# Performance work log

Measured on AMD Instinct MI355X. Metric: run time of the kernel, lower is better.

Reference implementation:

```python
import jax, jax.numpy as jnp
import numpy as np

BS, NQ, NTGT, NCLS, D = 16, 1024, 96, 4, 6
COST_CLASS, COST_BBOX = 1.0, 1.0
INF = jnp.float32(1e9)


def hungarian(cost):
    """Min-cost linear assignment (Jonker-Volgenant / e-maxx Hungarian).

    cost: (n, m) with n <= m. Returns (n,) int32: matched column for each row.
    Matches scipy.optimize.linear_sum_assignment's optimal assignment.
    """
    n, m = cost.shape
    # 1-indexed padded cost; row 0 / col 0 are virtual.
    a = jnp.zeros((n + 1, m + 1), jnp.float32).at[1:, 1:].set(cost.astype(jnp.float32))

    def assign_row(i, uvp):
        u, v, p = uvp  # p[j] = row matched to col j (0 = free)
        p = p.at[0].set(i)

        def dij_cond(c):
            _u, _v, _minv, _used, _way, j0 = c
            return p[j0] != 0

        def dij_body(c):
            u, v, minv, used, way, j0 = c
            used = used.at[j0].set(True)
            i0 = p[j0]
            cur = a[i0] - u[i0] - v                      # reduced costs, (m+1,)
            better = (cur < minv) & jnp.logical_not(used)
            minv = jnp.where(better, cur, minv)
            way = jnp.where(better, j0, way)
            masked = jnp.where(used, INF, minv)
            j1 = jnp.argmin(masked).astype(jnp.int32)
            delta = masked[j1]
            du = jnp.where(used, delta, jnp.float32(0))
            u = u.at[p].add(du)                          # u[p[j]] += delta for used j
            v = v - du
            minv = jnp.where(used, minv, minv - delta)
            return (u, v, minv, used, way, j1)

        minv0 = jnp.full(m + 1, INF, jnp.float32)
        used0 = jnp.zeros(m + 1, bool)
        way0 = jnp.zeros(m + 1, jnp.int32)
        u, v, _minv, _used, way, j0 = jax.lax.while_loop(
            dij_cond, dij_body, (u, v, minv0, used0, way0, jnp.int32(0)))

        def aug_cond(c):
            j0, _p = c
            return j0 != 0

        def aug_body(c):
            j0, p = c
            j1 = way[j0]
            p = p.at[j0].set(p[j1])
            return (j1, p)

        _, p = jax.lax.while_loop(aug_cond, aug_body, (j0, p))
        return (u, v, p)

    u0 = jnp.zeros(n + 1, jnp.float32)
    v0 = jnp.zeros(m + 1, jnp.float32)
    p0 = jnp.zeros(m + 1, jnp.int32)
    _, _, p = jax.lax.fori_loop(1, n + 1, assign_row, (u0, v0, p0))
    # invert: col4row[row] = col   (free cols / virtual col collapse into index 0)
    col4row = jnp.zeros(n + 1, jnp.int32).at[p[1:]].set(jnp.arange(1, m + 1, dtype=jnp.int32))
    return col4row[1:] - 1


def setup_inputs() -> dict:
    key = jax.random.key(0)
    k1, k2, k3, k4 = jax.random.split(key, 4)
    pred_logits = jax.random.normal(k1, (BS, NQ, NCLS), jnp.float32)
    pred_boxes = jax.random.uniform(k2, (BS, NQ, D), jnp.float32)
    labels = jax.random.randint(k3, (BS, NTGT), 0, NCLS, dtype=jnp.int32)
    control_points = jax.random.uniform(k4, (BS, NTGT, D), jnp.float32)
    return {"pred_logits": pred_logits, "pred_boxes": pred_boxes,
            "labels": labels, "control_points": control_points}


def reference(pred_logits, pred_boxes, labels, control_points):
    bs, nq, _ = pred_logits.shape
    ntgt = labels.shape[1]
    # cost matrix build (the memory-bound part)
    out_prob = jax.nn.softmax(pred_logits.reshape(bs * nq, -1), axis=-1)
    out_bbox = pred_boxes.reshape(bs * nq, -1)
    tgt_ids = labels.reshape(-1)
    tgt_bbox = control_points.reshape(bs * ntgt, -1)
    cost_class = -out_prob[:, tgt_ids]                              # (bs*nq, bs*ntgt)
    cost_bbox = jnp.abs(out_bbox[:, None, :] - tgt_bbox[None, :, :]).sum(-1)  # L1 cdist
    C = (COST_BBOX * cost_bbox + COST_CLASS * cost_class).reshape(bs, nq, bs * ntgt)

    # per-batch diagonal block -> Hungarian (targets as rows since ntgt <= nq)
    def per_batch(Cb, b):
        block = jax.lax.dynamic_slice(Cb, (0, b * ntgt), (nq, ntgt))  # (nq, ntgt)
        return hungarian(block.T)                                      # (ntgt,) matched query per target

    matched_query = jax.vmap(per_batch)(C, jnp.arange(bs, dtype=jnp.int32))
    return C, matched_query
```

## Files before the change

kernel.cpp:

```cpp
#include <hip/hip_runtime.h>


#define BSZ   16
#define NQ    1024
#define NTGT  96
#define NCLS  4
#define DD    6
#define NCOLS (BSZ * NTGT)
#define NROWS (BSZ * NQ)
#define LHINF 1e9f
#define NHB   16
#define ROWS_PER_BLK 8

typedef float f32x4 __attribute__((ext_vector_type(4)));

__device__ __forceinline__ float wave_fmin63(float x) {
    const int INF_I = __float_as_int(LHINF);
    int m;
    m = __builtin_amdgcn_update_dpp(INF_I, __float_as_int(x), 0x111, 0xf, 0xf, false);
    x = fminf(x, __int_as_float(m));
    m = __builtin_amdgcn_update_dpp(INF_I, __float_as_int(x), 0x112, 0xf, 0xf, false);
    x = fminf(x, __int_as_float(m));
    m = __builtin_amdgcn_update_dpp(INF_I, __float_as_int(x), 0x114, 0xf, 0xf, false);
    x = fminf(x, __int_as_float(m));
    m = __builtin_amdgcn_update_dpp(INF_I, __float_as_int(x), 0x118, 0xf, 0xf, false);
    x = fminf(x, __int_as_float(m));
    m = __builtin_amdgcn_update_dpp(INF_I, __float_as_int(x), 0x142, 0xf, 0xf, false);
    x = fminf(x, __int_as_float(m));
    m = __builtin_amdgcn_update_dpp(INF_I, __float_as_int(x), 0x143, 0xf, 0xf, false);
    x = fminf(x, __int_as_float(m));
    return x;
}

__device__ __forceinline__ float cost_elem6(const float* bx, const float* tv, float psel) {
    float cd = fabsf(bx[0] - tv[0]);
    cd += fabsf(bx[1] - tv[1]);
    cd += fabsf(bx[2] - tv[2]);
    cd += fabsf(bx[3] - tv[3]);
    cd += fabsf(bx[4] - tv[4]);
    cd += fabsf(bx[5] - tv[5]);
    return cd - psel;
}

__device__ __forceinline__ float4 softmax4(float4 lg) {
    const float mx = fmaxf(fmaxf(lg.x, lg.y), fmaxf(lg.z, lg.w));
    const float e0 = expf(lg.x - mx), e1 = expf(lg.y - mx);
    const float e2 = expf(lg.z - mx), e3 = expf(lg.w - mx);
    const float s = (e0 + e1) + (e2 + e3);
    return make_float4(e0 / s, e1 / s, e2 / s, e3 / s);
}

__global__ __launch_bounds__(256) void twsarg_kernel(
    const float* __restrict__ logits, const float* __restrict__ boxes,
    const int* __restrict__ labels, const float* __restrict__ tgt,
    float* __restrict__ tws, float* __restrict__ rowminv, int* __restrict__ rowarg)
{
    const int t = blockIdx.x;
    const int b = blockIdx.y;
    const int tr = b * NTGT + t;
    float tv[DD];
#pragma unroll
    for (int d = 0; d < DD; ++d) tv[d] = tgt[(size_t)tr * DD + d];
    const int cls = labels[tr];

    const int q4 = threadIdx.x * 4;
    const int row0 = b * NQ + q4;
    const float4* bx4 = (const float4*)(boxes + (size_t)row0 * DD);
    float bv[24];
#pragma unroll
    for (int c = 0; c < 6; ++c) {
        float4 f = bx4[c];
        bv[c * 4] = f.x; bv[c * 4 + 1] = f.y; bv[c * 4 + 2] = f.z; bv[c * 4 + 3] = f.w;
    }
    float o[4];
#pragma unroll
    for (int c = 0; c < 4; ++c) {
        const float4 p = softmax4(((const float4*)logits)[row0 + c]);
        const float ps = (cls == 0) ? p.x : (cls == 1) ? p.y : (cls == 2) ? p.z : p.w;
        o[c] = cost_elem6(bv + c * DD, tv, ps);
    }
    *((float4*)(tws + (size_t)tr * NQ + q4)) = make_float4(o[0], o[1], o[2], o[3]);

    float bvv = o[0]; int bj = q4;
    if (o[1] < bvv) { bvv = o[1]; bj = q4 + 1; }
    if (o[2] < bvv) { bvv = o[2]; bj = q4 + 2; }
    if (o[3] < bvv) { bvv = o[3]; bj = q4 + 3; }
#pragma unroll
    for (int off = 32; off > 0; off >>= 1) {
        const float ov = __shfl_down(bvv, off, 64);
        const int oj = __shfl_down(bj, off, 64);
        if (ov < bvv || (ov == bvv && oj < bj)) { bvv = ov; bj = oj; }
    }
    __shared__ float sv[4];
    __shared__ int sj[4];
    const int w = threadIdx.x >> 6;
    if ((threadIdx.x & 63) == 0) { sv[w] = bvv; sj[w] = bj; }
    __syncthreads();
    if (threadIdx.x == 0) {
        for (int i = 1; i < 4; ++i)
            if (sv[i] < bvv || (sv[i] == bvv && sj[i] < bj)) { bvv = sv[i]; bj = sj[i]; }
        rowminv[tr] = bvv; rowarg[tr] = bj;
    }
}

__global__ __launch_bounds__(384) void cost_kernel_fb(
    const float* __restrict__ logits, const float* __restrict__ boxes,
    const int* __restrict__ labels, const float* __restrict__ tgt,
    float* __restrict__ C)
{
    const int row = blockIdx.x;
    const int tid = threadIdx.x;
    const float4 pr = softmax4(*reinterpret_cast<const float4*>(logits + (size_t)row * NCLS));
    const float prr[4] = {pr.x, pr.y, pr.z, pr.w};
    float bx[DD];
#pragma unroll
    for (int d = 0; d < DD; ++d) bx[d] = boxes[(size_t)row * DD + d];
    const int colbase = tid * 4;
    const int4 lb = *reinterpret_cast<const int4*>(labels + colbase);
    const int cls[4] = {lb.x, lb.y, lb.z, lb.w};
    float tv[24];
    const float4* tg = reinterpret_cast<const float4*>(tgt + (size_t)colbase * DD);
#pragma unroll
    for (int d = 0; d < 6; ++d) {
        const float4 t4 = tg[d];
        tv[d * 4] = t4.x; tv[d * 4 + 1] = t4.y; tv[d * 4 + 2] = t4.z; tv[d * 4 + 3] = t4.w;
    }
    float o[4];
#pragma unroll
    for (int c = 0; c < 4; ++c) {
        const int cl = cls[c];
        const float ps = (cl == 0) ? prr[0] : (cl == 1) ? prr[1] : (cl == 2) ? prr[2] : prr[3];
        o[c] = cost_elem6(bx, tv + c * DD, ps);
    }
    *reinterpret_cast<float4*>(C + (size_t)row * NCOLS + colbase) =
        make_float4(o[0], o[1], o[2], o[3]);
}

__global__ __launch_bounds__(384) void fused_kernel(
    const float* __restrict__ tws, const float* __restrict__ logits,
    const float* __restrict__ boxes, const int* __restrict__ labels,
    const float* __restrict__ tgt,
    const float* __restrict__ rowminv, const int* __restrict__ rowarg,
    float* __restrict__ C, float* __restrict__ out_match, int warm)
{
    if (blockIdx.x >= NHB) {
        const int rb = (blockIdx.x - NHB) * ROWS_PER_BLK;
        const int tid = threadIdx.x;
        const int colbase = tid * 4;
        const int4 lb = ((const int4*)labels)[tid];
        const int cls[4] = {lb.x, lb.y, lb.z, lb.w};
        const float4* tg = (const float4*)(tgt + (size_t)colbase * DD);
        float tv[24];
#pragma unroll
        for (int c = 0; c < 6; ++c) {
            float4 f = tg[c];
            tv[c * 4] = f.x; tv[c * 4 + 1] = f.y; tv[c * 4 + 2] = f.z; tv[c * 4 + 3] = f.w;
        }
#pragma unroll
        for (int r = 0; r < ROWS_PER_BLK; ++r) {
            const int row = rb + r;
            const float4 pr = softmax4(((const float4*)logits)[row]);
            const float prr[4] = {pr.x, pr.y, pr.z, pr.w};
            const float* bp = boxes + (size_t)row * DD;
            float bx[DD];
#pragma unroll
            for (int d = 0; d < DD; ++d) bx[d] = bp[d];
            float o[4];
#pragma unroll
            for (int c = 0; c < 4; ++c) {
                const int cl = cls[c];
                const float ps = (cl == 0) ? prr[0] : (cl == 1) ? prr[1]
                               : (cl == 2) ? prr[2] : prr[3];
                o[c] = cost_elem6(bx, tv + c * DD, ps);
            }
            f32x4 ov;
            ov.x = o[0]; ov.y = o[1]; ov.z = o[2]; ov.w = o[3];
            __builtin_nontemporal_store(
                ov, (f32x4*)(C + (size_t)row * NCOLS + colbase));
        }
        return;
    }

    if (threadIdx.x >= 64) return;
    __builtin_amdgcn_s_setprio(2);
    const int b = blockIdx.x;
    const int lane = threadIdx.x;

    __shared__ float u_lds[NTGT + 1];
    __shared__ int   p_lds[NQ];
    __shared__ float dmark[NQ];
    __shared__ int   col_own[NQ];
    __shared__ int   ja_s[NTGT];
    __shared__ float um_s[NTGT];
    __shared__ int   pendf[NTGT];

    for (int t = lane; t < NQ; t += 64) { p_lds[t] = 0; col_own[t] = 0x7fffffff; }
    for (int t = lane; t < NTGT + 1; t += 64) u_lds[t] = 0.f;
    __builtin_amdgcn_wave_barrier();

    const int jbase = lane * 16;
    const float* Tb = tws + (size_t)b * NTGT * NQ;
    const float* Cstr = C + (size_t)b * NQ * NCOLS + b * NTGT;

    float v[16], Msel[16], msk[16];
    int way[16], p_reg[16];
#pragma unroll
    for (int k = 0; k < 16; ++k) v[k] = 0.f;

    if (warm) {
        for (int t = lane; t < NTGT; t += 64) {
            ja_s[t] = rowarg[b * NTGT + t];
            um_s[t] = rowminv[b * NTGT + t];
        }
        __builtin_amdgcn_wave_barrier();
        for (int t = lane; t < NTGT; t += 64)
            atomicMin(&col_own[ja_s[t]], t);
        __builtin_amdgcn_wave_barrier();
        for (int t = lane; t < NTGT; t += 64) {
            const int jt = ja_s[t];
            if (col_own[jt] == t) {
                p_lds[jt] = t + 1;
                u_lds[t + 1] = um_s[t];
                pendf[t] = 0;
            } else {
                pendf[t] = 1;
            }
        }
        __builtin_amdgcn_wave_barrier();
    } else {
        for (int t = lane; t < NTGT; t += 64) pendf[t] = 1;
        __builtin_amdgcn_wave_barrier();
    }

    for (int tt = 0; tt < NTGT; ++tt) {
        const int pending = __builtin_amdgcn_readfirstlane(pendf[tt]);
        if (!pending) continue;
        const int i = tt + 1;

        const int4* pl4 = (const int4*)(p_lds + jbase);
#pragma unroll
        for (int c = 0; c < 4; ++c) {
            int4 pp = pl4[c];
            p_reg[c * 4] = pp.x; p_reg[c * 4 + 1] = pp.y;
            p_reg[c * 4 + 2] = pp.z; p_reg[c * 4 + 3] = pp.w;
        }
#pragma unroll
        for (int k = 0; k < 16; ++k) { Msel[k] = LHINF; msk[k] = -LHINF; way[k] = 0; }
        unsigned used = 0u;
        int i0 = i; float Delta = 0.f; int j0cur = 0;
        bool domark = false; int markk = 0;
        float Dfinal = 0.f; int jfreem1 = 0;

        for (;;) {
            float av[16];
            if (warm) {
                const float4* rp = (const float4*)(Tb + (size_t)(i0 - 1) * NQ + jbase);
#pragma unroll
                for (int c = 0; c < 4; ++c) {
                    float4 f = rp[c];
                    av[c * 4] = f.x; av[c * 4 + 1] = f.y;
                    av[c * 4 + 2] = f.z; av[c * 4 + 3] = f.w;
                }
            } else {
                const float* cp = Cstr + (i0 - 1);
#pragma unroll
                for (int k = 0; k < 16; ++k) av[k] = cp[(size_t)(jbase + k) * NCOLS];
            }
            const float u_i0 = u_lds[i0];

#pragma unroll
            for (int k = 0; k < 16; ++k) {
                const bool mk = domark && (markk == k);
                Msel[k] = mk ? LHINF : Msel[k];
                msk[k]  = mk ? LHINF : msk[k];
            }
            used |= (domark ? (1u << markk) : 0u);

            const float c0 = Delta - u_i0;
            float lbv = LHINF; int lbk = 0; int lbp = 0;
#pragma unroll
            for (int k = 0; k < 16; ++k) {
                float cand = (av[k] - v[k]) + c0;
                cand = fmaxf(cand, msk[k]);
                const bool better = cand < Msel[k];
                way[k]  = better ? j0cur : way[k];
                Msel[k] = better ? cand : Msel[k];
                const bool b2 = Msel[k] < lbv;
                lbv = b2 ? Msel[k] : lbv;
                lbk = b2 ? k : lbk;
                lbp = b2 ? p_reg[k] : lbp;
            }
            const float red = wave_fmin63(lbv);
            const float gmin = __int_as_float(
                __builtin_amdgcn_readlane(__float_as_int(red), 63));
            const unsigned long long bal = __ballot(lbv == gmin);
            const int W = __builtin_amdgcn_readfirstlane((int)__builtin_ctzll(bal));
            const int lbjm1 = jbase + lbk;
            const int j1m1 = __builtin_amdgcn_readlane(lbjm1, W);
            const int i0n  = __builtin_amdgcn_readlane(lbp, W);
            const bool iswin = (lane == W);
            if (iswin) dmark[lbjm1] = lbv;
            domark = iswin; markk = lbk;
            if (i0n == 0) { Dfinal = gmin; jfreem1 = j1m1; break; }
            Delta = gmin; i0 = i0n; j0cur = j1m1 + 1;
        }

        __builtin_amdgcn_wave_barrier();
        float dmv[16];
        const float4* dm4 = (const float4*)(dmark + jbase);
#pragma unroll
        for (int c = 0; c < 4; ++c) {
            float4 f = dm4[c];
            dmv[c * 4] = f.x; dmv[c * 4 + 1] = f.y;
            dmv[c * 4 + 2] = f.z; dmv[c * 4 + 3] = f.w;
        }
#pragma unroll
        for (int k = 0; k < 16; ++k) {
            if ((used >> k) & 1u) {
                const float d = Dfinal - dmv[k];
                v[k] -= d;
                u_lds[p_reg[k]] += d;
            }
        }
        if (lane == 0) u_lds[i] += Dfinal;
        __builtin_amdgcn_wave_barrier();

        int j0m1 = jfreem1;
        for (;;) {
            const int kk = j0m1 & 15;
            const int owner = __builtin_amdgcn_readfirstlane(j0m1 >> 4);
            int s0 = (kk & 1) ? way[1]  : way[0];
            int s1 = (kk & 1) ? way[3]  : way[2];
            int s2 = (kk & 1) ? way[5]  : way[4];
            int s3 = (kk & 1) ? way[7]  : way[6];
            int s4 = (kk & 1) ? way[9]  : way[8];
            int s5 = (kk & 1) ? way[11] : way[10];
            int s6 = (kk & 1) ? way[13] : way[12];
            int s7 = (kk & 1) ? way[15] : way[14];
            int t0 = (kk & 2) ? s1 : s0;
            int t1 = (kk & 2) ? s3 : s2;
            int t2 = (kk & 2) ? s5 : s4;
            int t3 = (kk & 2) ? s7 : s6;
            int q0 = (kk & 4) ? t1 : t0;
            int q1 = (kk & 4) ? t3 : t2;
            int wsel = (kk & 8) ? q1 : q0;
            const int jn = __builtin_amdgcn_readlane(wsel, owner);
            const int pv = (jn == 0) ? i : p_lds[jn - 1];
            if (lane == 0) p_lds[j0m1] = pv;
            __builtin_amdgcn_wave_barrier();
            if (jn == 0) break;
            j0m1 = jn - 1;
        }
    }

    for (int t = lane; t < NQ; t += 64) {
        const int r = p_lds[t];
        if (r > 0) out_match[b * NTGT + r - 1] = (float)t;
    }
}

extern "C" void kernel_launch(void* const* d_in, const int* in_sizes, int n_in,
                              void* d_out, int out_size, void* d_ws, size_t ws_size,
                              hipStream_t stream) {
    const float* logits = (const float*)d_in[0];
    const float* boxes  = (const float*)d_in[1];
    const int*   labels = (const int*)d_in[2];
    const float* tgt    = (const float*)d_in[3];

    float* C = (float*)d_out;
    float* out_match = C + (size_t)NROWS * NCOLS;

    const size_t tws_e = (size_t)NCOLS * NQ;
    const size_t rmv_e = (size_t)NCOLS;
    const size_t need = (tws_e + rmv_e * 2) * sizeof(float);

    if (d_ws != nullptr && ws_size >= need) {
        float* tws     = (float*)d_ws;
        float* rowminv = tws + tws_e;
        int*   rowarg  = (int*)(rowminv + rmv_e);
        twsarg_kernel<<<dim3(NTGT, BSZ), 256, 0, stream>>>(
            logits, boxes, labels, tgt, tws, rowminv, rowarg);
        fused_kernel<<<NHB + NROWS / ROWS_PER_BLK, 384, 0, stream>>>(
            tws, logits, boxes, labels, tgt, rowminv, rowarg, C, out_match, 1);
    } else {
        cost_kernel_fb<<<NROWS, 384, 0, stream>>>(logits, boxes, labels, tgt, C);
        fused_kernel<<<NHB, 64, 0, stream>>>(
            nullptr, logits, boxes, labels, tgt, nullptr, nullptr, C, out_match, 0);
    }
}
```

Measured before the change: 167.7 us.

## Split fused cost-write/Hungarian kernel into separate sequential kernels

Breaks the fused kernel, which ran 16 Hungarian blocks alongside the C-writing blocks, into a standalone C-writing kernel followed by a separate Hungarian kernel launched with 64 threads per block. This removes the idle 320 threads and the priority hack in the Hungarian blocks, and lets the Hungarian waves run without competing for bandwidth or CUs with the C stores. In exchange it loses the overlap between the serial assignment work and the memory-bound C write, and adds a kernel launch.

```diff
diff --git a/kernel.cpp b/kernel.cpp
--- a/kernel.cpp
+++ b/kernel.cpp
@@ -9,7 +9,6 @@
 #define NCOLS (BSZ * NTGT)
 #define NROWS (BSZ * NQ)
 #define LHINF 1e9f
-#define NHB   16
 #define ROWS_PER_BLK 8
 
 typedef float f32x4 __attribute__((ext_vector_type(4)));
@@ -100,6 +99,47 @@
         for (int i = 1; i < 4; ++i)
             if (sv[i] < bvv || (sv[i] == bvv && sj[i] < bj)) { bvv = sv[i]; bj = sj[i]; }
         rowminv[tr] = bvv; rowarg[tr] = bj;
+    }
+}
+
+__global__ __launch_bounds__(384) void cwrite_kernel(
+    const float* __restrict__ logits, const float* __restrict__ boxes,
+    const int* __restrict__ labels, const float* __restrict__ tgt,
+    float* __restrict__ C)
+{
+    const int rb = blockIdx.x * ROWS_PER_BLK;
+    const int tid = threadIdx.x;
+    const int colbase = tid * 4;
+    const int4 lb = ((const int4*)labels)[tid];
+    const int cls[4] = {lb.x, lb.y, lb.z, lb.w};
+    const float4* tg = (const float4*)(tgt + (size_t)colbase * DD);
+    float tv[24];
+#pragma unroll
+    for (int c = 0; c < 6; ++c) {
+        float4 f = tg[c];
+        tv[c * 4] = f.x; tv[c * 4 + 1] = f.y; tv[c * 4 + 2] = f.z; tv[c * 4 + 3] = f.w;
+    }
+#pragma unroll
+    for (int r = 0; r < ROWS_PER_BLK; ++r) {
+        const int row = rb + r;
+        const float4 pr = softmax4(((const float4*)logits)[row]);
+        const float prr[4] = {pr.x, pr.y, pr.z, pr.w};
+        const float* bp = boxes + (size_t)row * DD;
+        float bx[DD];
+#pragma unroll
+        for (int d = 0; d < DD; ++d) bx[d] = bp[d];
+        float o[4];
+#pragma unroll
+        for (int c = 0; c < 4; ++c) {
+            const int cl = cls[c];
+            const float ps = (cl == 0) ? prr[0] : (cl == 1) ? prr[1]
+                           : (cl == 2) ? prr[2] : prr[3];
+            o[c] = cost_elem6(bx, tv + c * DD, ps);
+        }
+        f32x4 ov;
+        ov.x = o[0]; ov.y = o[1]; ov.z = o[2]; ov.w = o[3];
+        __builtin_nontemporal_store(
+            ov, (f32x4*)(C + (size_t)row * NCOLS + colbase));
     }
 }
 
@@ -136,53 +176,11 @@
         make_float4(o[0], o[1], o[2], o[3]);
 }
 
-__global__ __launch_bounds__(384) void fused_kernel(
-    const float* __restrict__ tws, const float* __restrict__ logits,
-    const float* __restrict__ boxes, const int* __restrict__ labels,
-    const float* __restrict__ tgt,
+__global__ __launch_bounds__(64) void hung_kernel(
+    const float* __restrict__ tws,
     const float* __restrict__ rowminv, const int* __restrict__ rowarg,
-    float* __restrict__ C, float* __restrict__ out_match, int warm)
+    const float* __restrict__ C, float* __restrict__ out_match, int warm)
 {
-    if (blockIdx.x >= NHB) {
-        const int rb = (blockIdx.x - NHB) * ROWS_PER_BLK;
-        const int tid = threadIdx.x;
-        const int colbase = tid * 4;
-        const int4 lb = ((const int4*)labels)[tid];
-        const int cls[4] = {lb.x, lb.y, lb.z, lb.w};
-        const float4* tg = (const float4*)(tgt + (size_t)colbase * DD);
-        float tv[24];
-#pragma unroll
-        for (int c = 0; c < 6; ++c) {
-            float4 f = tg[c];
-            tv[c * 4] = f.x; tv[c * 4 + 1] = f.y; tv[c * 4 + 2] = f.z; tv[c * 4 + 3] = f.w;
-        }
-#pragma unroll
-        for (int r = 0; r < ROWS_PER_BLK; ++r) {
-            const int row = rb + r;
-            const float4 pr = softmax4(((const float4*)logits)[row]);
-            const float prr[4] = {pr.x, pr.y, pr.z, pr.w};
-            const float* bp = boxes + (size_t)row * DD;
-            float bx[DD];
-#pragma unroll
-            for (int d = 0; d < DD; ++d) bx[d] = bp[d];
-            float o[4];
-#pragma unroll
-            for (int c = 0; c < 4; ++c) {
-                const int cl = cls[c];
-                const float ps = (cl == 0) ? prr[0] : (cl == 1) ? prr[1]
-                               : (cl == 2) ? prr[2] : prr[3];
-                o[c] = cost_elem6(bx, tv + c * DD, ps);
-            }
-            f32x4 ov;
-            ov.x = o[0]; ov.y = o[1]; ov.z = o[2]; ov.w = o[3];
-            __builtin_nontemporal_store(
-                ov, (f32x4*)(C + (size_t)row * NCOLS + colbase));
-        }
-        return;
-    }
-
-    if (threadIdx.x >= 64) return;
-    __builtin_amdgcn_s_setprio(2);
     const int b = blockIdx.x;
     const int lane = threadIdx.x;
 
@@ -380,11 +378,13 @@
         int*   rowarg  = (int*)(rowminv + rmv_e);
         twsarg_kernel<<<dim3(NTGT, BSZ), 256, 0, stream>>>(
             logits, boxes, labels, tgt, tws, rowminv, rowarg);
-        fused_kernel<<<NHB + NROWS / ROWS_PER_BLK, 384, 0, stream>>>(
-            tws, logits, boxes, labels, tgt, rowminv, rowarg, C, out_match, 1);
+        cwrite_kernel<<<NROWS / ROWS_PER_BLK, 384, 0, stream>>>(
+            logits, boxes, labels, tgt, C);
+        hung_kernel<<<BSZ, 64, 0, stream>>>(
+            tws, rowminv, rowarg, C, out_match, 1);
     } else {
         cost_kernel_fb<<<NROWS, 384, 0, stream>>>(logits, boxes, labels, tgt, C);
-        fused_kernel<<<NHB, 64, 0, stream>>>(
-            nullptr, logits, boxes, labels, tgt, nullptr, nullptr, C, out_match, 0);
-    }
-}
+        hung_kernel<<<BSZ, 64, 0, stream>>>(
+            nullptr, nullptr, nullptr, C, out_match, 0);
+    }
+}
```

New measurement: 196.9 us. +17.5%, slower.
